# Performance work log

Measured on AMD Instinct MI355X. Metric: run time of the kernel, lower is better.

Reference implementation:

```python
import jax, jax.numpy as jnp
import numpy as np

B, C, T = 16, 256, 2048
K = 1024  # codes per layer
N_LAYERS = 3


def setup_inputs() -> dict:
    key = jax.random.key(0)
    kx, k0, k1, k2 = jax.random.split(key, 4)
    x = jax.random.normal(kx, (B, C, T), dtype=jnp.float32)
    scale = 1.0 / K
    emb0 = jax.random.uniform(k0, (K, C), minval=-scale, maxval=scale, dtype=jnp.float32)
    emb1 = jax.random.uniform(k1, (K, C), minval=-scale, maxval=scale, dtype=jnp.float32)
    emb2 = jax.random.uniform(k2, (K, C), minval=-scale, maxval=scale, dtype=jnp.float32)
    return {"x": x, "emb0": emb0, "emb1": emb1, "emb2": emb2}


def _vq_layer(x, emb):
    # x: [B, C, T], emb: [K, C]
    b, c, t = x.shape
    flat = jnp.transpose(x, (0, 2, 1)).reshape(-1, c)          # [B*T, C]
    # squared L2 distance to each code: ||f||^2 - 2 f.e + ||e||^2
    dist = (jnp.sum(flat * flat, axis=1, keepdims=True)
            - 2.0 * flat @ emb.T
            + jnp.sum(emb * emb, axis=1))                       # [B*T, K]
    idx = jnp.argmin(dist, axis=1)                              # [B*T]
    quant = jnp.transpose(emb[idx].reshape(b, t, c), (0, 2, 1)) # [B, C, T]
    sg = jax.lax.stop_gradient
    loss = jnp.mean((sg(quant) - x) ** 2) + jnp.mean((quant - sg(x)) ** 2)
    quantized = x + sg(quant - x)  # straight-through
    return quantized, loss


def reference(x, emb0, emb1, emb2):
    total_loss = jnp.float32(0.0)
    out = x
    for emb in (emb0, emb1, emb2):
        out, loss = _vq_layer(out, emb)
        total_loss = total_loss + loss
    return out, total_loss
```

## Files before the change

### kernel.cpp

```cpp
#include <hip/hip_runtime.h>
#include <stdint.h>

#define B_  16
#define C_  256
#define T_  2048
#define K_  1024
#define TOTAL_ELEMS 8388608

typedef short bf16x8 __attribute__((ext_vector_type(8)));
typedef float f32x4 __attribute__((ext_vector_type(4)));

__device__ __forceinline__ unsigned long long pack_key(float d, int idx) {
  unsigned u = __float_as_uint(d);
  u = (u & 0x80000000u) ? ~u : (u | 0x80000000u);
  return ((unsigned long long)u << 32) | (unsigned)idx;
}
__device__ __forceinline__ float unpack_dist(unsigned long long key) {
  unsigned du = (unsigned)(key >> 32);
  unsigned bits = (du & 0x80000000u) ? (du ^ 0x80000000u) : ~du;
  return __uint_as_float(bits);
}

__device__ __forceinline__ unsigned short f2bf_rne(float f) {
  unsigned u = __float_as_uint(f);
  unsigned r = u + 0x7FFFu + ((u >> 16) & 1u);
  return (unsigned short)(r >> 16);
}

__device__ __forceinline__ void gload_lds16(const void* g, void* l) {
  __builtin_amdgcn_global_load_lds(
      (const __attribute__((address_space(1))) unsigned int*)g,
      (__attribute__((address_space(3))) unsigned int*)l, 16, 0, 0);
}

__global__ __launch_bounds__(256) void prep_kernel(
    const float* __restrict__ e0, const float* __restrict__ e1,
    const float* __restrict__ e2, float* __restrict__ nrm,
    unsigned short* __restrict__ ebf, uint4* __restrict__ keysM_region,
    float* __restrict__ loss_accum) {
  int bid = blockIdx.x;
  int tid = threadIdx.x;
  if (bid < 12) {
    int i = bid * 256 + tid;
    const float* e = (i < 1024) ? e0 : (i < 2048) ? e1 : e2;
    const float* p = e + (size_t)(i & 1023) * C_;
    float s = 0.0f;
    for (int c = 0; c < C_; c += 4) {
      float4 v = *(const float4*)(p + c);
      s = fmaf(v.x, v.x, s); s = fmaf(v.y, v.y, s);
      s = fmaf(v.z, v.z, s); s = fmaf(v.w, v.w, s);
    }
    nrm[i] = s;
  } else if (bid < 268) {
    int i = (bid - 12) * 256 + tid;
    float4 v = *(const float4*)(e0 + (size_t)i * 4);
    unsigned lo = (unsigned)f2bf_rne(v.x) | ((unsigned)f2bf_rne(v.y) << 16);
    unsigned hi = (unsigned)f2bf_rne(v.z) | ((unsigned)f2bf_rne(v.w) << 16);
    *(uint2*)(ebf + (size_t)i * 4) = make_uint2(lo, hi);
  } else {
    int i = (bid - 268) * 256 + tid;
    keysM_region[i] = make_uint4(0xFFFFFFFFu, 0xFFFFFFFFu, 0xFFFFFFFFu, 0xFFFFFFFFu);
    if (bid == 268 && tid == 0) *loss_accum = 0.0f;
  }
}

__global__ __launch_bounds__(256) void xpose_kernel(
    const float* __restrict__ x, unsigned short* __restrict__ xT,
    float* __restrict__ loss_accum) {
  __shared__ float ftile[64][68];
  __shared__ float red[4];
  int tid = threadIdx.x;
  int bid = blockIdx.x;
  int b  = bid >> 7;
  int t0 = ((bid >> 2) & 31) << 6;
  int c0 = (bid & 3) << 6;
  int cr = tid >> 4;
  int t_loc = (tid & 15) * 4;
  const float* src = x + (size_t)b * (C_ * T_) + (size_t)c0 * T_ + t0;
  float sq = 0.0f;
#pragma unroll
  for (int q = 0; q < 4; q++) {
    int c_loc = cr + q * 16;
    float4 v = *(const float4*)(src + (size_t)c_loc * T_ + t_loc);
    *(float4*)&ftile[c_loc][t_loc] = v;
    sq = fmaf(v.x, v.x, sq); sq = fmaf(v.y, v.y, sq);
    sq = fmaf(v.z, v.z, sq); sq = fmaf(v.w, v.w, sq);
  }
  for (int off = 32; off > 0; off >>= 1) sq += __shfl_down(sq, off, 64);
  if ((tid & 63) == 0) red[tid >> 6] = sq;
  __syncthreads();
  if (tid == 0)
    atomicAdd(loss_accum, red[0] + red[1] + red[2] + red[3]);

  int t_row = tid >> 2;
  int cs = (tid & 3) * 16;
  unsigned pk[8];
#pragma unroll
  for (int i = 0; i < 8; i++) {
    unsigned short lo = f2bf_rne(ftile[cs + 2 * i][t_row]);
    unsigned short hi = f2bf_rne(ftile[cs + 2 * i + 1][t_row]);
    pk[i] = (unsigned)lo | ((unsigned)hi << 16);
  }
  unsigned short* dst = xT + ((size_t)(b * T_ + t0 + t_row) * C_ + c0 + cs);
  *(uint4*)dst       = make_uint4(pk[0], pk[1], pk[2], pk[3]);
  *((uint4*)dst + 1) = make_uint4(pk[4], pk[5], pk[6], pk[7]);
}

__global__ __launch_bounds__(256) void map_tile_kernel(
    const float* __restrict__ e0, const float* __restrict__ e1,
    const float* __restrict__ e2, const float* __restrict__ nrm,
    unsigned long long* __restrict__ keysM) {
  __shared__ float As[16][68];
  __shared__ float Bs[16][68];
  int bid = blockIdx.x;
  int m = bid >> 8;
  int tb = bid & 255;
  int ar0 = (tb >> 4) << 6;
  int br0 = (tb & 15) << 6;
  const float* Ap = m ? e1 : e0;
  const float* Bp = m ? e2 : e1;
  const float* nB = nrm + (m + 1) * 1024;

  int tid = threadIdx.x;
  int ty = tid >> 4, tx = tid & 15;
  int srow = tid >> 2;
  int skp  = (tid & 3) << 2;

  float acc[4][4];
#pragma unroll
  for (int i = 0; i < 4; i++)
#pragma unroll
    for (int j = 0; j < 4; j++) acc[i][j] = 0.0f;

  const float* gA = Ap + (size_t)(ar0 + srow) * C_ + skp;
  const float* gB = Bp + (size_t)(br0 + srow) * C_ + skp;

  for (int kk = 0; kk < C_; kk += 16) {
    float4 av = *(const float4*)(gA + kk);
    float4 bv = *(const float4*)(gB + kk);
    __syncthreads();
    As[skp + 0][srow] = av.x; As[skp + 1][srow] = av.y;
    As[skp + 2][srow] = av.z; As[skp + 3][srow] = av.w;
    Bs[skp + 0][srow] = bv.x; Bs[skp + 1][srow] = bv.y;
    Bs[skp + 2][srow] = bv.z; Bs[skp + 3][srow] = bv.w;
    __syncthreads();
#pragma unroll
    for (int k = 0; k < 16; k++) {
      float4 a4 = *(const float4*)&As[k][ty * 4];
      float4 b4 = *(const float4*)&Bs[k][tx * 4];
      float aa[4] = {a4.x, a4.y, a4.z, a4.w};
      float bb[4] = {b4.x, b4.y, b4.z, b4.w};
#pragma unroll
      for (int i = 0; i < 4; i++)
#pragma unroll
        for (int j = 0; j < 4; j++)
          acc[i][j] = fmaf(aa[i], bb[j], acc[i][j]);
    }
  }

  float nv[4];
#pragma unroll
  for (int j = 0; j < 4; j++) nv[j] = nB[br0 + tx * 4 + j];

#pragma unroll
  for (int i = 0; i < 4; i++) {
    unsigned long long best = 0xFFFFFFFFFFFFFFFFULL;
#pragma unroll
    for (int j = 0; j < 4; j++) {
      int code = br0 + tx * 4 + j;
      float s = nv[j] - 2.0f * acc[i][j];
      unsigned long long key = pack_key(s, code);
      if (key < best) best = key;
    }
#pragma unroll
    for (int off = 1; off < 16; off <<= 1) {
      unsigned long long o = __shfl_xor(best, off, 64);
      if (o < best) best = o;
    }
    if (tx == 0)
      atomicMin(&keysM[m * 1024 + ar0 + ty * 4 + i], best);
  }
}

__global__ __launch_bounds__(256, 1) void l0_mfma_kernel(
    const unsigned short* __restrict__ xT, const unsigned short* __restrict__ ebf,
    const float* __restrict__ e0n, unsigned long long* __restrict__ keys) {
  extern __shared__ char smem[];
  char* Abuf = smem;
  char* Bbuf = smem + 65536;

  int tid = threadIdx.x;
  int l = tid & 63, w = tid >> 6;
  int wr = w >> 1, wc = w & 1;
  int row0 = blockIdx.x << 7;
  int lr = l & 15, lg = l >> 4;

  {
    char* abase = Abuf + w * 16384;
    int q = (l & 31) >> 2;
    int s = l & 3;
    int rsub = l >> 5;
#pragma unroll
    for (int i = 0; i < 16; i++) {
      int row = w * 32 + i * 2 + rsub;
      int kelem = (((q ^ ((row >> 2) & 1)) << 5) + ((s ^ (row & 3)) << 3));
      gload_lds16(xT + (((size_t)(row0 + row)) << 8) + kelem, abase + i * 1024);
    }
  }

#define STAGEB(d, p, kk) do {                                            \
    char* bbase = Bbuf + (d) * 16384 + w * 4096;                         \
    _Pragma("unroll")                                                    \
    for (int i_ = 0; i_ < 4; i_++) {                                     \
      int code_ = (p) * 256 + w * 64 + i_ * 16 + (l >> 2);               \
      int kelem_ = ((kk) << 5) + (((l & 3) ^ (code_ & 3)) << 3);         \
      gload_lds16(ebf + (((size_t)code_) << 8) + kelem_, bbase + i_ * 1024); \
    } } while (0)

  f32x4 acc[2][4][4];
  float bestv[4][4];
  int   bestm[4][4];
#pragma unroll
  for (int mi = 0; mi < 4; mi++)
#pragma unroll
    for (int r = 0; r < 4; r++) { bestv[mi][r] = -1e30f; bestm[mi][r] = 0; }

  STAGEB(0, 0, 0);
  __syncthreads();

  int aseg = (lg ^ (lr & 3)) << 4;
  int akb1 = (lr >> 2) & 1;
  int d = 0;
  for (int p = 0; p < 4; p++) {
#pragma unroll
    for (int c01 = 0; c01 < 2; c01++)
#pragma unroll
      for (int ni = 0; ni < 4; ni++) {
        float iv = -0.5f * e0n[p * 256 + c01 * 128 + wc * 64 + ni * 16 + lr];
        f32x4 ivv = {iv, iv, iv, iv};
#pragma unroll
        for (int mi = 0; mi < 4; mi++) acc[c01][mi][ni] = ivv;
      }
#pragma unroll
    for (int kk = 0; kk < 8; kk++) {
      if (kk < 7) { STAGEB(d ^ 1, p, kk + 1); }
      else if (p < 3) { STAGEB(d ^ 1, p + 1, 0); }
      bf16x8 aF[4], bF[2][4];
#pragma unroll
      for (int mi = 0; mi < 4; mi++)
        aF[mi] = *(const bf16x8*)(Abuf + (wr * 64 + mi * 16 + lr) * 512 +
                                  ((kk ^ akb1) << 6) + aseg);
#pragma unroll
      for (int c01 = 0; c01 < 2; c01++)
#pragma unroll
        for (int ni = 0; ni < 4; ni++)
          bF[c01][ni] = *(const bf16x8*)(Bbuf + d * 16384 +
                        (c01 * 128 + wc * 64 + ni * 16 + lr) * 64 + aseg);
#pragma unroll
      for (int c01 = 0; c01 < 2; c01++)
#pragma unroll
        for (int mi = 0; mi < 4; mi++)
#pragma unroll
          for (int ni = 0; ni < 4; ni++)
            acc[c01][mi][ni] = __builtin_amdgcn_mfma_f32_16x16x32_bf16(
                aF[mi], bF[c01][ni], acc[c01][mi][ni], 0, 0, 0);
      __syncthreads();
      d ^= 1;
    }
    int pm = p * 8;
#pragma unroll
    for (int mi = 0; mi < 4; mi++)
#pragma unroll
      for (int r = 0; r < 4; r++)
#pragma unroll
        for (int c01 = 0; c01 < 2; c01++)
#pragma unroll
          for (int ni = 0; ni < 4; ni++) {
            float v = acc[c01][mi][ni][r];
            if (v > bestv[mi][r]) { bestv[mi][r] = v; bestm[mi][r] = pm + c01 * 4 + ni; }
          }
  }
#undef STAGEB

  unsigned long long (*kred)[2] = (unsigned long long(*)[2])Bbuf;
#pragma unroll
  for (int mi = 0; mi < 4; mi++)
#pragma unroll
    for (int r = 0; r < 4; r++) {
      float sdist = -2.0f * bestv[mi][r];
      int m = bestm[mi][r];
      int code = ((m >> 3) << 8) | (((m >> 2) & 1) << 7) | (wc << 6) |
                 ((m & 3) << 4) | lr;
      unsigned long long key = pack_key(sdist, code);
#pragma unroll
      for (int off = 1; off < 16; off <<= 1) {
        unsigned long long o = __shfl_xor(key, off, 64);
        if (o < key) key = o;
      }
      if (lr == 0) kred[wr * 64 + mi * 16 + lg * 4 + r][wc] = key;
    }
  __syncthreads();
  if (tid < 128) {
    unsigned long long a = kred[tid][0], b = kred[tid][1];
    keys[row0 + tid] = a < b ? a : b;
  }
}

__global__ __launch_bounds__(256) void finish_kernel(
    const float* __restrict__ emb2,
    const unsigned long long* __restrict__ keys,
    const unsigned long long* __restrict__ keysM,
    const float* __restrict__ nrm,
    float* __restrict__ out, float* __restrict__ loss_accum) {
  __shared__ int code2_l[64];
  __shared__ float rloss[64];
  int tid = threadIdx.x;
  int b  = blockIdx.x >> 5;
  int t0 = (blockIdx.x & 31) << 6;
  int tt = tid & 63, w = tid >> 6;

  if (w == 0) {
    unsigned long long key0 = keys[(size_t)b * T_ + t0 + tt];
    int idx0 = (int)(key0 & 0xFFFFFFFFULL);
    float s0 = unpack_dist(key0);
    unsigned long long k1 = keysM[idx0];
    int c1 = (int)(k1 & 0xFFFFFFFFULL);
    unsigned long long k2 = keysM[1024 + c1];
    code2_l[tt] = (int)(k2 & 0xFFFFFFFFULL);
    rloss[tt] = s0 + nrm[idx0] + unpack_dist(k1) + nrm[1024 + c1] + unpack_dist(k2);
  }
  __syncthreads();

  float* ob = out + ((size_t)b << 19);
  int code2 = code2_l[tt];
  const float* e2row = emb2 + (size_t)code2 * C_;
  for (int c4 = w * 64; c4 < w * 64 + 64; c4 += 4) {
    float4 ev = *(const float4*)(e2row + c4);
    float evv[4] = {ev.x, ev.y, ev.z, ev.w};
#pragma unroll
    for (int u = 0; u < 4; u++)
      ob[(size_t)(c4 + u) * T_ + t0 + tt] = evv[u];
  }
  if (w == 0) {
    float tot = rloss[tt];
    for (int off = 32; off > 0; off >>= 1)
      tot += __shfl_down(tot, off, 64);
    if (tt == 0) atomicAdd(loss_accum, tot);
  }
}

__global__ void finalize_kernel(const float* __restrict__ loss_accum,
                                float* __restrict__ out_loss) {
  *out_loss = 2.0f * (*loss_accum) / 8388608.0f;
}

extern "C" void kernel_launch(void* const* d_in, const int* in_sizes, int n_in,
                              void* d_out, int out_size, void* d_ws, size_t ws_size,
                              hipStream_t stream) {
  const float* x  = (const float*)d_in[0];
  const float* e0 = (const float*)d_in[1];
  const float* e1 = (const float*)d_in[2];
  const float* e2 = (const float*)d_in[3];
  float* out = (float*)d_out;
  char* ws = (char*)d_ws;

  unsigned long long* keys  = (unsigned long long*)ws;
  unsigned long long* keysM = (unsigned long long*)(ws + 262144);
  float* nrm  = (float*)(ws + 278528);
  float* loss_accum = (float*)(ws + 290816);
  unsigned short* embbf = (unsigned short*)(ws + 294912);
  unsigned short* xT    = (unsigned short*)(ws + 819200);

  prep_kernel<<<272, 256, 0, stream>>>(e0, e1, e2, nrm, embbf, (uint4*)keysM, loss_accum);
  xpose_kernel<<<2048, 256, 0, stream>>>(x, xT, loss_accum);
  l0_mfma_kernel<<<256, 256, 98304, stream>>>(xT, embbf, nrm, keys);
  map_tile_kernel<<<512, 256, 0, stream>>>(e0, e1, e2, nrm, keysM);
  finish_kernel<<<512, 256, 0, stream>>>(e2, keys, keysM, nrm, out, loss_accum);
  finalize_kernel<<<1, 1, 0, stream>>>(loss_accum, out + TOTAL_ELEMS);
}
```

Baseline: 110.7 us.

## Fuse transpose into layer-0 MFMA kernel and fold finalize into finish

The separate transpose kernel is removed. The layer-0 MFMA kernel now reads x directly, converts it to bf16, writes it into swizzled LDS and accumulates the sum of squares for the loss. The kernel moves to 512 threads (8 waves, each covering 64 codes per pass) with a matching B-staging swizzle and a 4-way key reduction. The finalize kernel is replaced by a last-block atomic counter in finish_kernel. This removes the xT global round trip and two launches, but the fused prologue now serialises x loading before the MFMA loop inside each block.

```diff
diff --git a/kernel.cpp b/kernel.cpp
--- a/kernel.cpp
+++ b/kernel.cpp
@@ -37,7 +37,7 @@
     const float* __restrict__ e0, const float* __restrict__ e1,
     const float* __restrict__ e2, float* __restrict__ nrm,
     unsigned short* __restrict__ ebf, uint4* __restrict__ keysM_region,
-    float* __restrict__ loss_accum) {
+    float* __restrict__ loss_accum, unsigned* __restrict__ counter) {
   int bid = blockIdx.x;
   int tid = threadIdx.x;
   if (bid < 12) {
@@ -60,50 +60,8 @@
   } else {
     int i = (bid - 268) * 256 + tid;
     keysM_region[i] = make_uint4(0xFFFFFFFFu, 0xFFFFFFFFu, 0xFFFFFFFFu, 0xFFFFFFFFu);
-    if (bid == 268 && tid == 0) *loss_accum = 0.0f;
-  }
-}
-
-__global__ __launch_bounds__(256) void xpose_kernel(
-    const float* __restrict__ x, unsigned short* __restrict__ xT,
-    float* __restrict__ loss_accum) {
-  __shared__ float ftile[64][68];
-  __shared__ float red[4];
-  int tid = threadIdx.x;
-  int bid = blockIdx.x;
-  int b  = bid >> 7;
-  int t0 = ((bid >> 2) & 31) << 6;
-  int c0 = (bid & 3) << 6;
-  int cr = tid >> 4;
-  int t_loc = (tid & 15) * 4;
-  const float* src = x + (size_t)b * (C_ * T_) + (size_t)c0 * T_ + t0;
-  float sq = 0.0f;
-#pragma unroll
-  for (int q = 0; q < 4; q++) {
-    int c_loc = cr + q * 16;
-    float4 v = *(const float4*)(src + (size_t)c_loc * T_ + t_loc);
-    *(float4*)&ftile[c_loc][t_loc] = v;
-    sq = fmaf(v.x, v.x, sq); sq = fmaf(v.y, v.y, sq);
-    sq = fmaf(v.z, v.z, sq); sq = fmaf(v.w, v.w, sq);
-  }
-  for (int off = 32; off > 0; off >>= 1) sq += __shfl_down(sq, off, 64);
-  if ((tid & 63) == 0) red[tid >> 6] = sq;
-  __syncthreads();
-  if (tid == 0)
-    atomicAdd(loss_accum, red[0] + red[1] + red[2] + red[3]);
-
-  int t_row = tid >> 2;
-  int cs = (tid & 3) * 16;
-  unsigned pk[8];
-#pragma unroll
-  for (int i = 0; i < 8; i++) {
-    unsigned short lo = f2bf_rne(ftile[cs + 2 * i][t_row]);
-    unsigned short hi = f2bf_rne(ftile[cs + 2 * i + 1][t_row]);
-    pk[i] = (unsigned)lo | ((unsigned)hi << 16);
-  }
-  unsigned short* dst = xT + ((size_t)(b * T_ + t0 + t_row) * C_ + c0 + cs);
-  *(uint4*)dst       = make_uint4(pk[0], pk[1], pk[2], pk[3]);
-  *((uint4*)dst + 1) = make_uint4(pk[4], pk[5], pk[6], pk[7]);
+    if (bid == 268 && tid == 0) { *loss_accum = 0.0f; *counter = 0u; }
+  }
 }
 
 __global__ __launch_bounds__(256) void map_tile_kernel(
@@ -182,42 +140,75 @@
   }
 }
 
-__global__ __launch_bounds__(256, 1) void l0_mfma_kernel(
-    const unsigned short* __restrict__ xT, const unsigned short* __restrict__ ebf,
-    const float* __restrict__ e0n, unsigned long long* __restrict__ keys) {
+__global__ __launch_bounds__(512, 2) void l0_fused_kernel(
+    const float* __restrict__ x, const unsigned short* __restrict__ ebf,
+    const float* __restrict__ e0n, unsigned long long* __restrict__ keys,
+    float* __restrict__ loss_accum) {
   extern __shared__ char smem[];
   char* Abuf = smem;
   char* Bbuf = smem + 65536;
 
   int tid = threadIdx.x;
   int l = tid & 63, w = tid >> 6;
-  int wr = w >> 1, wc = w & 1;
   int row0 = blockIdx.x << 7;
+
+  {
+    int row = tid & 127;
+    int cg  = tid >> 7;
+    int bb  = blockIdx.x >> 4;
+    int t0  = (blockIdx.x & 15) << 7;
+    const float* xb = x + (size_t)bb * (C_ * T_) + t0 + row;
+    float sumsq = 0.0f;
+#pragma unroll
+    for (int i = 0; i < 8; i++) {
+      int c0 = cg * 64 + i * 8;
+      float v[8];
+#pragma unroll
+      for (int u = 0; u < 8; u++) {
+        v[u] = xb[(size_t)(c0 + u) * T_];
+        sumsq = fmaf(v[u], v[u], sumsq);
+      }
+      unsigned pk[4];
+#pragma unroll
+      for (int j = 0; j < 4; j++)
+        pk[j] = (unsigned)f2bf_rne(v[2 * j]) | ((unsigned)f2bf_rne(v[2 * j + 1]) << 16);
+      int cc = c0 >> 3;
+      char* dst = Abuf + row * 512 + ((((cc >> 2)) ^ ((row >> 2) & 1)) << 6) +
+                  (((cc & 3) ^ (row & 3)) << 4);
+      *(uint4*)dst = make_uint4(pk[0], pk[1], pk[2], pk[3]);
+    }
+    for (int off = 32; off > 0; off >>= 1) sumsq += __shfl_down(sumsq, off, 64);
+    float* red = (float*)(Bbuf + 16384);
+    if (l == 0) red[w] = sumsq;
+    __syncthreads();
+    if (tid == 0) {
+      float s = 0.0f;
+#pragma unroll
+      for (int i = 0; i < 8; i++) s += red[i];
+      atomicAdd(loss_accum, s);
+    }
+  }
+
+#define STAGEB(d_, p_, kk_) do {                                             \
+    char* bbase = Bbuf + (d_) * 16384 + (w * 32) * 64;                       \
+    _Pragma("unroll")                                                        \
+    for (int j_ = 0; j_ < 2; j_++) {                                         \
+      int code_ = (p_) * 256 + w * 32 + j_ * 16 + (l >> 2);                  \
+      int seg_ = (l & 3) ^ ((l >> 2) & 3) ^ ((l >> 4) & 3);                  \
+      gload_lds16(ebf + (((size_t)code_) << 8) + ((kk_) << 5) + (seg_ << 3), \
+                  bbase + j_ * 1024);                                        \
+    } } while (0)
+
+  STAGEB(0, 0, 0);
+  __syncthreads();
+
+  int wr = w >> 2, wc = w & 3;
   int lr = l & 15, lg = l >> 4;
-
-  {
-    char* abase = Abuf + w * 16384;
-    int q = (l & 31) >> 2;
-    int s = l & 3;
-    int rsub = l >> 5;
-#pragma unroll
-    for (int i = 0; i < 16; i++) {
-      int row = w * 32 + i * 2 + rsub;
-      int kelem = (((q ^ ((row >> 2) & 1)) << 5) + ((s ^ (row & 3)) << 3));
-      gload_lds16(xT + (((size_t)(row0 + row)) << 8) + kelem, abase + i * 1024);
-    }
-  }
-
-#define STAGEB(d, p, kk) do {                                            \
-    char* bbase = Bbuf + (d) * 16384 + w * 4096;                         \
-    _Pragma("unroll")                                                    \
-    for (int i_ = 0; i_ < 4; i_++) {                                     \
-      int code_ = (p) * 256 + w * 64 + i_ * 16 + (l >> 2);               \
-      int kelem_ = ((kk) << 5) + (((l & 3) ^ (code_ & 3)) << 3);         \
-      gload_lds16(ebf + (((size_t)code_) << 8) + kelem_, bbase + i_ * 1024); \
-    } } while (0)
-
-  f32x4 acc[2][4][4];
+  int akb1 = (lr >> 2) & 1;
+  int asegoff = (lg ^ (lr & 3)) << 4;
+  int bsegoff = (lg ^ ((lr ^ (lr >> 2)) & 3)) << 4;
+
+  f32x4 acc[4][4];
   float bestv[4][4];
   int   bestm[4][4];
 #pragma unroll
@@ -225,72 +216,57 @@
 #pragma unroll
     for (int r = 0; r < 4; r++) { bestv[mi][r] = -1e30f; bestm[mi][r] = 0; }
 
-  STAGEB(0, 0, 0);
-  __syncthreads();
-
-  int aseg = (lg ^ (lr & 3)) << 4;
-  int akb1 = (lr >> 2) & 1;
   int d = 0;
   for (int p = 0; p < 4; p++) {
 #pragma unroll
-    for (int c01 = 0; c01 < 2; c01++)
-#pragma unroll
-      for (int ni = 0; ni < 4; ni++) {
-        float iv = -0.5f * e0n[p * 256 + c01 * 128 + wc * 64 + ni * 16 + lr];
-        f32x4 ivv = {iv, iv, iv, iv};
-#pragma unroll
-        for (int mi = 0; mi < 4; mi++) acc[c01][mi][ni] = ivv;
-      }
+    for (int ni = 0; ni < 4; ni++) {
+      float iv = -0.5f * e0n[p * 256 + wc * 64 + ni * 16 + lr];
+      f32x4 ivv = {iv, iv, iv, iv};
+#pragma unroll
+      for (int mi = 0; mi < 4; mi++) acc[mi][ni] = ivv;
+    }
 #pragma unroll
     for (int kk = 0; kk < 8; kk++) {
       if (kk < 7) { STAGEB(d ^ 1, p, kk + 1); }
       else if (p < 3) { STAGEB(d ^ 1, p + 1, 0); }
-      bf16x8 aF[4], bF[2][4];
+      bf16x8 aF[4], bF[4];
 #pragma unroll
       for (int mi = 0; mi < 4; mi++)
         aF[mi] = *(const bf16x8*)(Abuf + (wr * 64 + mi * 16 + lr) * 512 +
-                                  ((kk ^ akb1) << 6) + aseg);
-#pragma unroll
-      for (int c01 = 0; c01 < 2; c01++)
+                                  ((kk ^ akb1) << 6) + asegoff);
+#pragma unroll
+      for (int ni = 0; ni < 4; ni++)
+        bF[ni] = *(const bf16x8*)(Bbuf + d * 16384 +
+                                  (wc * 64 + ni * 16 + lr) * 64 + bsegoff);
+#pragma unroll
+      for (int mi = 0; mi < 4; mi++)
 #pragma unroll
         for (int ni = 0; ni < 4; ni++)
-          bF[c01][ni] = *(const bf16x8*)(Bbuf + d * 16384 +
-                        (c01 * 128 + wc * 64 + ni * 16 + lr) * 64 + aseg);
-#pragma unroll
-      for (int c01 = 0; c01 < 2; c01++)
-#pragma unroll
-        for (int mi = 0; mi < 4; mi++)
-#pragma unroll
-          for (int ni = 0; ni < 4; ni++)
-            acc[c01][mi][ni] = __builtin_amdgcn_mfma_f32_16x16x32_bf16(
-                aF[mi], bF[c01][ni], acc[c01][mi][ni], 0, 0, 0);
+          acc[mi][ni] = __builtin_amdgcn_mfma_f32_16x16x32_bf16(
+              aF[mi], bF[ni], acc[mi][ni], 0, 0, 0);
       __syncthreads();
       d ^= 1;
     }
-    int pm = p * 8;
 #pragma unroll
     for (int mi = 0; mi < 4; mi++)
 #pragma unroll
       for (int r = 0; r < 4; r++)
 #pragma unroll
-        for (int c01 = 0; c01 < 2; c01++)
-#pragma unroll
-          for (int ni = 0; ni < 4; ni++) {
-            float v = acc[c01][mi][ni][r];
-            if (v > bestv[mi][r]) { bestv[mi][r] = v; bestm[mi][r] = pm + c01 * 4 + ni; }
-          }
+        for (int ni = 0; ni < 4; ni++) {
+          float v = acc[mi][ni][r];
+          if (v > bestv[mi][r]) { bestv[mi][r] = v; bestm[mi][r] = p * 4 + ni; }
+        }
   }
 #undef STAGEB
 
-  unsigned long long (*kred)[2] = (unsigned long long(*)[2])Bbuf;
+  unsigned long long (*kred)[4] = (unsigned long long(*)[4])Bbuf;
 #pragma unroll
   for (int mi = 0; mi < 4; mi++)
 #pragma unroll
     for (int r = 0; r < 4; r++) {
       float sdist = -2.0f * bestv[mi][r];
       int m = bestm[mi][r];
-      int code = ((m >> 3) << 8) | (((m >> 2) & 1) << 7) | (wc << 6) |
-                 ((m & 3) << 4) | lr;
+      int code = ((m >> 2) << 8) | (wc << 6) | ((m & 3) << 4) | lr;
       unsigned long long key = pack_key(sdist, code);
 #pragma unroll
       for (int off = 1; off < 16; off <<= 1) {
@@ -301,8 +277,11 @@
     }
   __syncthreads();
   if (tid < 128) {
-    unsigned long long a = kred[tid][0], b = kred[tid][1];
-    keys[row0 + tid] = a < b ? a : b;
+    unsigned long long b0 = kred[tid][0], b1 = kred[tid][1];
+    unsigned long long b2 = kred[tid][2], b3 = kred[tid][3];
+    if (b1 < b0) b0 = b1;
+    if (b3 < b2) b2 = b3;
+    keys[row0 + tid] = b0 < b2 ? b0 : b2;
   }
 }
 
@@ -311,7 +290,8 @@
     const unsigned long long* __restrict__ keys,
     const unsigned long long* __restrict__ keysM,
     const float* __restrict__ nrm,
-    float* __restrict__ out, float* __restrict__ loss_accum) {
+    float* __restrict__ out, float* __restrict__ loss_accum,
+    unsigned* __restrict__ counter) {
   __shared__ int code2_l[64];
   __shared__ float rloss[64];
   int tid = threadIdx.x;
@@ -347,11 +327,14 @@
       tot += __shfl_down(tot, off, 64);
     if (tt == 0) atomicAdd(loss_accum, tot);
   }
-}
-
-__global__ void finalize_kernel(const float* __restrict__ loss_accum,
-                                float* __restrict__ out_loss) {
-  *out_loss = 2.0f * (*loss_accum) / 8388608.0f;
+  if (tid == 0) {
+    __threadfence();
+    unsigned old = atomicAdd(counter, 1u);
+    if (old == 511u) {
+      float L = atomicAdd(loss_accum, 0.0f);
+      out[TOTAL_ELEMS] = 2.0f * L / 8388608.0f;
+    }
+  }
 }
 
 extern "C" void kernel_launch(void* const* d_in, const int* in_sizes, int n_in,
@@ -368,13 +351,12 @@
   unsigned long long* keysM = (unsigned long long*)(ws + 262144);
   float* nrm  = (float*)(ws + 278528);
   float* loss_accum = (float*)(ws + 290816);
+  unsigned* counter = (unsigned*)(ws + 290820);
   unsigned short* embbf = (unsigned short*)(ws + 294912);
-  unsigned short* xT    = (unsigned short*)(ws + 819200);
-
-  prep_kernel<<<272, 256, 0, stream>>>(e0, e1, e2, nrm, embbf, (uint4*)keysM, loss_accum);
-  xpose_kernel<<<2048, 256, 0, stream>>>(x, xT, loss_accum);
-  l0_mfma_kernel<<<256, 256, 98304, stream>>>(xT, embbf, nrm, keys);
+
+  prep_kernel<<<272, 256, 0, stream>>>(e0, e1, e2, nrm, embbf, (uint4*)keysM,
+                                       loss_accum, counter);
+  l0_fused_kernel<<<256, 512, 98304, stream>>>(x, embbf, nrm, keys, loss_accum);
   map_tile_kernel<<<512, 256, 0, stream>>>(e0, e1, e2, nrm, keysM);
-  finish_kernel<<<512, 256, 0, stream>>>(e2, keys, keysM, nrm, out, loss_accum);
-  finalize_kernel<<<1, 1, 0, stream>>>(loss_accum, out + TOTAL_ELEMS);
-}
+  finish_kernel<<<512, 256, 0, stream>>>(e2, keys, keysM, nrm, out, loss_accum, counter);
+}
```

Result: faster. 92.49 us (-16.4%).
